# Kernel tuning notes

Hardware: AMD Instinct MI355X
Metric: run time of the kernel (lower is better)

Reference implementation:

```python
import jax, jax.numpy as jnp
import numpy as np

GROUPS = 4
EPS = 1e-5


def conv1d(x, w, b):
    # x [B,Cin,NA,T], w [Cout,Cin,1,K], 'same' padding along T
    K = w.shape[-1]
    pad = (K - 1) // 2
    y = jax.lax.conv_general_dilated(x, w, (1, 1), [(0, 0), (pad, pad)],
                                     dimension_numbers=('NCHW', 'OIHW', 'NCHW'))
    return y + b[None, :, None, None]


def group_norm(x, g, b):
    B, C, H, W = x.shape
    xg = x.reshape(B, GROUPS, C // GROUPS, H, W)
    m = xg.mean((2, 3, 4), keepdims=True)
    v = xg.var((2, 3, 4), keepdims=True)
    xn = ((xg - m) * jax.lax.rsqrt(v + EPS)).reshape(B, C, H, W)
    return xn * g[None, :, None, None] + b[None, :, None, None]


def avg_pool_t(x, k):
    B, C, H, T = x.shape
    return x.reshape(B, C, H, T // k, k).mean(-1)


def branch(x, w1, b1, g1, be1, w2, b2, g2, be2):
    y = avg_pool_t(jax.nn.gelu(group_norm(conv1d(x, w1, b1), g1, be1), approximate=False), 2)
    y = avg_pool_t(jax.nn.gelu(group_norm(conv1d(y, w2, b2), g2, be2), approximate=False), 4)
    # B C NA T -> B NA (T C)
    B, C, NA, T = y.shape
    return jnp.transpose(y, (0, 2, 3, 1)).reshape(B, NA, T * C)


def rvq(feat, cbs):
    # feat [B,NA,D]; cbs [nq,V,D] -> residual vector quantization
    def step(res, cb):
        d = (res * res).sum(-1, keepdims=True) \
            - 2.0 * jnp.einsum('bnd,vd->bnv', res, cb) \
            + (cb * cb).sum(-1)              # [B,NA,V]
        idx = jnp.argmin(d, axis=-1)          # [B,NA]
        q = cb[idx]                           # gather [B,NA,D]
        return res - q, (q, idx)
    _, (qs, idxs) = jax.lax.scan(step, feat, cbs)
    return qs.sum(0), idxs                    # [B,NA,D], [nq,B,NA]


def reference(x, w11, w12, w13, w14, b1, g1, be1,
              w21, w22, w23, w24, b2, g2, be2, codebooks):
    B, N, A, T = x.shape
    xc = x.reshape(B, N * A, T)[:, None]  # [B,1,NA,T]
    feats = jnp.stack([
        branch(xc, w11, b1[0], g1[0], be1[0], w21, b2[0], g2[0], be2[0]),
        branch(xc, w12, b1[1], g1[1], be1[1], w22, b2[1], g2[1], be2[1]),
        branch(xc, w13, b1[2], g1[2], be1[2], w23, b2[2], g2[2], be2[2]),
        branch(xc, w14, b1[3], g1[3], be1[3], w24, b2[3], g2[3], be2[3]),
    ])  # [4,B,NA,D]
    quant, idxs = jax.vmap(rvq)(feats, codebooks)  # [4,B,NA,D], [4,nq,B,NA]
    # straight-through estimator
    out = feats + jax.lax.stop_gradient(quant - feats)
    return out, idxs


def setup_inputs() -> dict:
    key = jax.random.key(0)
    ks = jax.random.split(key, 16)
    C = 8
    d = {
        'x': jax.random.normal(ks[0], (8, 32, 4, 200), jnp.float32),
        'w11': jax.random.normal(ks[1], (C, 1, 1, 21), jnp.float32) * 0.1,
        'w12': jax.random.normal(ks[2], (C, 1, 1, 15), jnp.float32) * 0.1,
        'w13': jax.random.normal(ks[3], (C, 1, 1, 9), jnp.float32) * 0.1,
        'w14': jax.random.normal(ks[4], (C, 1, 1, 5), jnp.float32) * 0.1,
        'b1': jnp.zeros((4, C), jnp.float32),
        'g1': jnp.ones((4, C), jnp.float32),
        'be1': jnp.zeros((4, C), jnp.float32),
        'w21': jax.random.normal(ks[5], (C, C, 1, 9), jnp.float32) * 0.1,
        'w22': jax.random.normal(ks[6], (C, C, 1, 7), jnp.float32) * 0.1,
        'w23': jax.random.normal(ks[7], (C, C, 1, 5), jnp.float32) * 0.1,
        'w24': jax.random.normal(ks[8], (C, C, 1, 3), jnp.float32) * 0.1,
        'b2': jnp.zeros((4, C), jnp.float32),
        'g2': jnp.ones((4, C), jnp.float32),
        'be2': jnp.zeros((4, C), jnp.float32),
        'codebooks': jax.random.normal(ks[9], (4, 8, 8192, 200), jnp.float32) * 0.5,
    }
    return d
```

## Files before the change

kernel.cpp:

```cpp
#include <hip/hip_runtime.h>
#include <hip/hip_bf16.h>
#include <math.h>

#define NBR 4
#define BB 8
#define NAA 128
#define T_IN 200
#define CCH 8
#define NQ 8
#define NV 8192
#define DD 200
#define ROWS 1024
#define KPAD 224
#define NKG 28
#define CBQSH ((size_t)NBR*NKG*NV*8)

typedef __attribute__((ext_vector_type(8))) short short8;
typedef __attribute__((ext_vector_type(4))) float f32x4;

__device__ __forceinline__ unsigned short f2bf(float x) {
  unsigned u = __float_as_uint(x);
  unsigned r = (u + 0x7fffu + ((u >> 16) & 1u)) >> 16;
  return (unsigned short)r;
}
__device__ __forceinline__ bool lexlt(float av, int ai, float bv, int bi) {
  return (av < bv) || (av == bv && ai < bi);
}
__device__ __forceinline__ unsigned umn(unsigned a, unsigned b) { return a < b ? a : b; }
__device__ __forceinline__ unsigned umx(unsigned a, unsigned b) { return a > b ? a : b; }
__device__ __forceinline__ unsigned skey(float s, int idx) {
  unsigned u = __float_as_uint(s);
  unsigned mask = ((unsigned)((int)u >> 31)) | 0x80000000u;
  return ((u ^ mask) & 0xFFFFE000u) | (unsigned)idx;
}
__device__ __forceinline__ void gld16(const short* g, short* s) {
  __builtin_amdgcn_global_load_lds(
      (const __attribute__((address_space(1))) unsigned*)g,
      (__attribute__((address_space(3))) unsigned*)s, 16, 0, 0);
}

template<int K>
__device__ __forceinline__ void conv1_stats_body(
    const float* __restrict__ sx, const float* __restrict__ wr, float bias,
    int tl, double& s, double& s2)
{
  constexpr int pad = (K-1)/2;
  if (tl < 25) {
    int t0 = 8*tl;
    float xw[K+7];
    #pragma unroll
    for (int i = 0; i < K+7; ++i) {
      int xi = t0 - pad + i;
      xw[i] = ((unsigned)xi < (unsigned)T_IN) ? sx[xi] : 0.f;
    }
    #pragma unroll
    for (int m = 0; m < 8; ++m) {
      float acc = bias;
      #pragma unroll
      for (int k = 0; k < K; ++k)
        acc = fmaf(wr[k], xw[m + k], acc);
      s += acc; s2 += (double)acc * acc;
    }
  }
}

__global__ __launch_bounds__(256) void k_conv1_stats(
    const float* __restrict__ x,
    const float* __restrict__ w11, const float* __restrict__ w12,
    const float* __restrict__ w13, const float* __restrict__ w14,
    const float* __restrict__ b1,
    double* __restrict__ partS, double* __restrict__ partQ)
{
  const int bid = blockIdx.x;
  const int br = bid >> 10;
  const int b  = (bid >> 7) & 7;
  const int na = bid & 127;
  const int tid = threadIdx.x;
  const int c  = tid >> 5;
  const int tl = tid & 31;
  const float* w = (br==0) ? w11 : (br==1) ? w12 : (br==2) ? w13 : w14;

  __shared__ float sx[T_IN];
  if (tid < T_IN) sx[tid] = x[((size_t)b*NAA + na)*T_IN + tid];
  __syncthreads();

  const float bias = b1[br*CCH + c];
  double s = 0.0, s2 = 0.0;
  switch (br) {
    case 0: conv1_stats_body<21>(sx, w + c*21, bias, tl, s, s2); break;
    case 1: conv1_stats_body<15>(sx, w + c*15, bias, tl, s, s2); break;
    case 2: conv1_stats_body<9> (sx, w + c*9,  bias, tl, s, s2); break;
    default: conv1_stats_body<5>(sx, w + c*5,  bias, tl, s, s2); break;
  }
  __shared__ double rs[256], rq[256];
  rs[tid] = s; rq[tid] = s2;
  __syncthreads();
  for (int off = 32; off > 0; off >>= 1) {
    if ((tid & 63) < off) { rs[tid] += rs[tid+off]; rq[tid] += rq[tid+off]; }
    __syncthreads();
  }
  if ((tid & 63) == 0) {
    int g = tid >> 6;
    int pi = (((br*BB + b)*4 + g) << 7) + na;
    partS[pi] = rs[tid]; partQ[pi] = rq[tid];
  }
}

template<int K1, int K2>
__device__ __forceinline__ void mid_body(
    const float* __restrict__ sx, float* __restrict__ sy,
    const float* __restrict__ w1, const float* __restrict__ w2,
    float bias1, float fm, float rst, float gm, float bt, float bias2,
    int c, int tl, float* __restrict__ yout, double& s, double& s2)
{
  constexpr int pad1 = (K1-1)/2, pad2 = (K2-1)/2;
  const float* wr = w1 + c*K1;
  if (tl < 25) {
    int t0 = 8*tl;
    float xw[K1+7];
    #pragma unroll
    for (int i = 0; i < K1+7; ++i) {
      int xi = t0 - pad1 + i;
      xw[i] = ((unsigned)xi < (unsigned)T_IN) ? sx[xi] : 0.f;
    }
    #pragma unroll
    for (int m = 0; m < 4; ++m) {
      float u = 0.f;
      #pragma unroll
      for (int h = 0; h < 2; ++h) {
        float acc = bias1;
        #pragma unroll
        for (int k = 0; k < K1; ++k)
          acc = fmaf(wr[k], xw[2*m + h + k], acc);
        float xn = (acc - fm) * rst * gm + bt;
        u += 0.5f * xn * (1.0f + erff(xn * 0.70710678118654752440f));
      }
      sy[c*100 + 4*tl + m] = 0.5f * u;
    }
  }
  __syncthreads();
  if (tl < 25) {
    int t0 = 4*tl;
    float a0 = bias2, a1 = bias2, a2 = bias2, a3 = bias2;
    #pragma unroll
    for (int cin = 0; cin < CCH; ++cin) {
      const float* wr2 = w2 + (c*CCH + cin)*K2;
      float wv[K2];
      #pragma unroll
      for (int k = 0; k < K2; ++k) wv[k] = wr2[k];
      float yw[K2+3];
      #pragma unroll
      for (int i = 0; i < K2+3; ++i) {
        int yi = t0 - pad2 + i;
        yw[i] = ((unsigned)yi < 100u) ? sy[cin*100 + yi] : 0.f;
      }
      #pragma unroll
      for (int k = 0; k < K2; ++k) a0 = fmaf(wv[k], yw[k], a0);
      #pragma unroll
      for (int k = 0; k < K2; ++k) a1 = fmaf(wv[k], yw[1 + k], a1);
      #pragma unroll
      for (int k = 0; k < K2; ++k) a2 = fmaf(wv[k], yw[2 + k], a2);
      #pragma unroll
      for (int k = 0; k < K2; ++k) a3 = fmaf(wv[k], yw[3 + k], a3);
    }
    *(float4*)&yout[t0] = make_float4(a0, a1, a2, a3);
    s += a0; s2 += (double)a0 * a0;
    s += a1; s2 += (double)a1 * a1;
    s += a2; s2 += (double)a2 * a2;
    s += a3; s2 += (double)a3 * a3;
  }
}

__global__ __launch_bounds__(256) void k_mid(
    const float* __restrict__ x,
    const float* __restrict__ w11, const float* __restrict__ w12,
    const float* __restrict__ w13, const float* __restrict__ w14,
    const float* __restrict__ b1, const float* __restrict__ g1,
    const float* __restrict__ be1,
    const double* __restrict__ partS1, const double* __restrict__ partQ1,
    const float* __restrict__ w21, const float* __restrict__ w22,
    const float* __restrict__ w23, const float* __restrict__ w24,
    const float* __restrict__ b2,
    float* __restrict__ y2raw,
    double* __restrict__ partS, double* __restrict__ partQ)
{
  const int bid = blockIdx.x;
  const int br = bid >> 10;
  const int b  = (bid >> 7) & 7;
  const int na = bid & 127;
  const int tid = threadIdx.x;
  const int c  = tid >> 5;
  const int tl = tid & 31;
  const int wid = tid >> 6;
  const int l = tid & 63;
  const float* w1 = (br==0) ? w11 : (br==1) ? w12 : (br==2) ? w13 : w14;
  const float* w2 = (br==0) ? w21 : (br==1) ? w22 : (br==2) ? w23 : w24;

  __shared__ float sx[T_IN];
  __shared__ float sy[CCH*100];
  __shared__ float sstat[8];
  if (tid < T_IN) sx[tid] = x[((size_t)b*NAA + na)*T_IN + tid];

  {
    int base = (((br*BB + b)*4 + wid) << 7);
    double a  = partS1[base + l] + partS1[base + 64 + l];
    double qn = partQ1[base + l] + partQ1[base + 64 + l];
    #pragma unroll
    for (int m = 32; m >= 1; m >>= 1) {
      a  += __shfl_xor(a, m);
      qn += __shfl_xor(qn, m);
    }
    if (l == 0) {
      double mean = a / 51200.0;
      double var  = qn / 51200.0 - mean*mean;
      sstat[wid*2]     = (float)mean;
      sstat[wid*2 + 1] = (float)(1.0 / sqrt(var + 1e-5));
    }
  }
  __syncthreads();

  const float bias1 = b1[br*CCH + c];
  const float fm  = sstat[(c>>1)*2];
  const float rst = sstat[(c>>1)*2 + 1];
  const float gm = g1[br*CCH + c], bt = be1[br*CCH + c];
  const float bias2 = b2[br*CCH + c];
  float* yout = y2raw + ((((size_t)br*BB + b)*CCH + c)*NAA + na)*100;

  double s = 0.0, s2 = 0.0;
  switch (br) {
    case 0: mid_body<21,9>(sx, sy, w1, w2, bias1, fm, rst, gm, bt, bias2, c, tl, yout, s, s2); break;
    case 1: mid_body<15,7>(sx, sy, w1, w2, bias1, fm, rst, gm, bt, bias2, c, tl, yout, s, s2); break;
    case 2: mid_body<9,5> (sx, sy, w1, w2, bias1, fm, rst, gm, bt, bias2, c, tl, yout, s, s2); break;
    default: mid_body<5,3>(sx, sy, w1, w2, bias1, fm, rst, gm, bt, bias2, c, tl, yout, s, s2); break;
  }

  __shared__ double rs[256], rq[256];
  rs[tid] = s; rq[tid] = s2;
  __syncthreads();
  for (int off = 32; off > 0; off >>= 1) {
    if ((tid & 63) < off) { rs[tid] += rs[tid+off]; rq[tid] += rq[tid+off]; }
    __syncthreads();
  }
  if ((tid & 63) == 0) {
    int g = tid >> 6;
    int pi = (((br*BB + b)*4 + g) << 7) + na;
    partS[pi] = rs[tid]; partQ[pi] = rq[tid];
  }
}

__global__ __launch_bounds__(256) void k_tail(
    const float* __restrict__ y2raw, const float* __restrict__ g2,
    const float* __restrict__ be2,
    const double* __restrict__ partS2, const double* __restrict__ partQ2,
    float* __restrict__ res, short* __restrict__ resh)
{
  const int tid = threadIdx.x;
  int idx = blockIdx.x * 256 + tid;
  int c  = idx & 7;
  int tp = (idx >> 3) % 25;
  int na = (idx / 200) & 127;
  int b  = (idx / 25600) & 7;
  int br = idx / 204800;
  const int wid = tid >> 6, l = tid & 63;

  if (idx < NBR*3*ROWS*8) {
    int pos = idx & 7;
    int prow = (idx >> 3) & 1023;
    int r2  = idx >> 13;
    int pbr = r2 / 3, kgp = r2 - pbr*3;
    resh[(((size_t)pbr*NKG + 25 + kgp)*ROWS + prow)*8 + pos] = 0;
  }

  __shared__ float sstat[8];
  {
    int base = (((br*BB + b)*4 + wid) << 7);
    double a  = partS2[base + l] + partS2[base + 64 + l];
    double qn = partQ2[base + l] + partQ2[base + 64 + l];
    #pragma unroll
    for (int m = 32; m >= 1; m >>= 1) {
      a  += __shfl_xor(a, m);
      qn += __shfl_xor(qn, m);
    }
    if (l == 0) {
      double mean = a / 25600.0;
      double var  = qn / 25600.0 - mean*mean;
      sstat[wid*2]     = (float)mean;
      sstat[wid*2 + 1] = (float)(1.0 / sqrt(var + 1e-5));
    }
  }
  __syncthreads();

  int g = c >> 1;
  float fm  = sstat[g*2];
  float rst = sstat[g*2 + 1];
  float gm = g2[br*CCH + c], bt = be2[br*CCH + c];
  float4 v = *(const float4*)&y2raw[((((size_t)br*BB + b)*CCH + c)*NAA + na)*100 + 4*tp];
  float sum4 = 0.f;
  #pragma unroll
  for (int h = 0; h < 4; ++h) {
    float xv = (h==0) ? v.x : (h==1) ? v.y : (h==2) ? v.z : v.w;
    float xn = (xv - fm) * rst * gm + bt;
    sum4 += 0.5f * xn * (1.0f + erff(xn * 0.70710678118654752440f));
  }
  float val = 0.25f * sum4;
  int row = b*NAA + na;
  res[((size_t)br*ROWS + row)*DD + tp*8 + c] = val;
  resh[(((size_t)br*NKG + tp)*ROWS + row)*8 + c] = (short)f2bf(val);
}

__global__ __launch_bounds__(256) void k_cvt_cb(
    const float* __restrict__ cbs, int q0, int nq,
    short* __restrict__ dh, float* __restrict__ cbn)
{
  __shared__ short S[25][65][8];
  const int blk = blockIdx.x;
  const int vt = blk & 127;
  const int t  = blk >> 7;
  const int br = t / nq, ql = t - br*nq;
  const int q = q0 + ql;
  const int tid = threadIdx.x;
  const int row = tid >> 2, fq = tid & 3;
  const int v0 = vt*64;
  const float* srow = cbs + ((size_t)(br*NQ + q)*NV + v0 + row)*DD;

  float s = 0.f;
  for (int j = 0; j < 13; ++j) {
    int f4 = fq + 4*j;
    if (f4 < 50) {
      float4 f = *(const float4*)&srow[4*f4];
      s += f.x*f.x + f.y*f.y + f.z*f.z + f.w*f.w;
      *(short4*)&S[f4>>1][row][(f4&1)*4] =
          make_short4((short)f2bf(f.x), (short)f2bf(f.y),
                      (short)f2bf(f.z), (short)f2bf(f.w));
    }
  }
  s += __shfl_xor(s, 1);
  s += __shfl_xor(s, 2);
  if (fq == 0) cbn[(size_t)(br*NQ + q)*NV + v0 + row] = s;
  __syncthreads();

  short* dq = dh + (size_t)ql*CBQSH;
  for (int u = tid; u < NKG*64*2; u += 256) {
    int kg = u >> 7;
    int rem = u & 127;
    int v = rem >> 1, pos = (rem & 1)*4;
    short4 val = (kg < 25) ? *(const short4*)&S[kg][v][pos]
                           : make_short4(0,0,0,0);
    *(short4*)&dq[(((size_t)br*NKG + kg)*NV + v0 + v)*8 + pos] = val;
  }
}

__global__ __launch_bounds__(256) void k_gemm(
    const short* __restrict__ resh, const short* __restrict__ cbh,
    const float* __restrict__ cbn, int q,
    unsigned* __restrict__ candk)
{
  __shared__ short S[2][4][130][8];

  const int p = blockIdx.x;
  const int x = p & 7;
  const int sIdx = p >> 3;
  const int br = sIdx >> 6;
  const int rb = (sIdx >> 3) & 7;
  const int vb = x*8 + (sIdx & 7);
  const int tid = threadIdx.x;
  const int w = tid >> 6;
  const int l = tid & 63;
  const int wr = w >> 1, wc = w & 1;
  const int kgl = l >> 4, fr = l & 15;

  f32x4 acc[4][4];
  #pragma unroll
  for (int i = 0; i < 4; ++i)
    #pragma unroll
    for (int j = 0; j < 4; ++j)
      acc[i][j] = (f32x4){0.f, 0.f, 0.f, 0.f};

  short8 aA[2][4];

  #define STAGE(nb, ks)                                                         \
    {                                                                           \
      _Pragma("unroll")                                                         \
      for (int i = 0; i < 4; ++i)                                               \
        aA[nb][i] = *(const short8*)&resh[                                      \
          (((size_t)br*NKG + (ks)*4 + kgl)*ROWS + rb*128 + wr*64 + i*16 + fr)*8]; \
      _Pragma("unroll")                                                         \
      for (int t = 0; t < 2; ++t) {                                             \
        int u = (w << 1) | t;                                                   \
        int kg = u >> 1, wh = u & 1;                                            \
        gld16(cbh + (((size_t)br*NKG + (ks)*4 + kg)*NV + vb*128 + wh*64 + l)*8, \
              &S[nb][kg][wh*64][0]);                                            \
      }                                                                         \
    }

  STAGE(0, 0);

  #pragma unroll
  for (int ks = 0; ks < 7; ++ks) {
    const int cur = ks & 1, nxt = cur ^ 1;
    if (ks < 6) {
      STAGE(nxt, ks + 1);
      asm volatile("s_waitcnt vmcnt(6)" ::: "memory");
    } else {
      asm volatile("s_waitcnt vmcnt(0)" ::: "memory");
    }
    __builtin_amdgcn_s_barrier();

    short8 bh[4];
    #pragma unroll
    for (int j = 0; j < 4; ++j)
      bh[j] = *(const short8*)&S[cur][kgl][wc*64 + j*16 + fr][0];
    #pragma unroll
    for (int i = 0; i < 4; ++i)
      #pragma unroll
      for (int j = 0; j < 4; ++j)
        acc[i][j] = __builtin_amdgcn_mfma_f32_16x16x32_bf16(aA[cur][i], bh[j], acc[i][j], 0, 0, 0);

    asm volatile("" ::: "memory");
    __builtin_amdgcn_s_barrier();
  }

  const float* cn = cbn + (size_t)(br*NQ + q)*NV;
  float nj[4]; int vgj[4];
  #pragma unroll
  for (int j = 0; j < 4; ++j) {
    vgj[j] = vb*128 + wc*64 + j*16 + fr;
    nj[j] = 0.5f * cn[vgj[j]];
  }
  #pragma unroll
  for (int i = 0; i < 4; ++i) {
    #pragma unroll
    for (int reg = 0; reg < 4; ++reg) {
      unsigned k0 = skey(nj[0] - acc[i][0][reg], vgj[0]);
      unsigned k1 = skey(nj[1] - acc[i][1][reg], vgj[1]);
      unsigned k2 = skey(nj[2] - acc[i][2][reg], vgj[2]);
      unsigned k3 = skey(nj[3] - acc[i][3][reg], vgj[3]);
      unsigned a = umn(k0, k1), b = umx(k0, k1);
      unsigned c = umn(k2, k3), d = umx(k2, k3);
      unsigned c1 = umn(a, c);
      unsigned c2 = umn(umx(a, c), umn(b, d));
      #pragma unroll
      for (int m = 1; m <= 8; m <<= 1) {
        unsigned o1 = __shfl_xor(c1, m);
        unsigned o2 = __shfl_xor(c2, m);
        unsigned t = umx(c1, o1);
        c1 = umn(c1, o1);
        c2 = umn(umn(t, c2), o2);
      }
      if (fr == 0) {
        int grow = br*ROWS + rb*128 + wr*64 + i*16 + kgl*4 + reg;
        size_t o = ((size_t)grow*64 + vb)*4 + wc*2;
        candk[o] = c1; candk[o+1] = c2;
      }
    }
  }
  #undef STAGE
}

__global__ __launch_bounds__(256) void k_update3(
    const float* __restrict__ cbs, const float* __restrict__ cbn,
    const unsigned* __restrict__ candk,
    float* __restrict__ res, float* __restrict__ outq,
    float* __restrict__ outi, short* __restrict__ resh, int q)
{
  const int wid = threadIdx.x >> 6;
  const int lane = threadIdx.x & 63;
  const int r = blockIdx.x*4 + wid;
  const int br = r >> 10;
  const int row = r & 1023;

  const unsigned* ck = candk + (size_t)r * 256;
  uint4 kk = *(const uint4*)&ck[4*lane];
  unsigned c0 = kk.x, c1 = kk.y, c2 = kk.z, c3 = kk.w;

  unsigned mykey = 0xFFFFFFFFu;
  #pragma unroll
  for (int t = 0; t < 8; ++t) {
    unsigned lm = umn(umn(c0, c1), umn(c2, c3));
    #pragma unroll
    for (int m = 1; m <= 32; m <<= 1)
      lm = umn(lm, __shfl_xor(lm, m));
    if (c0 == lm) c0 = 0xFFFFFFFFu;
    if (c1 == lm) c1 = 0xFFFFFFFFu;
    if (c2 == lm) c2 = 0xFFFFFFFFu;
    if (c3 == lm) c3 = 0xFFFFFFFFu;
    if ((lane >> 3) == t) mykey = lm;
  }
  const int mycand = (int)(mykey & 0x1FFFu);

  const int kl = lane & 7;
  const float* cbrow = cbs + ((size_t)(br*NQ + q)*NV + mycand)*DD;
  const float* rrow0 = res + (size_t)r*DD;
  float dot = 0.f;
  #pragma unroll
  for (int u = 0; u < 7; ++u) {
    int f4 = kl + 8*u;
    if (f4 < 50) {
      float4 r4 = *(const float4*)&rrow0[4*f4];
      float4 c4 = *(const float4*)&cbrow[4*f4];
      dot = fmaf(r4.x, c4.x, dot);
      dot = fmaf(r4.y, c4.y, dot);
      dot = fmaf(r4.z, c4.z, dot);
      dot = fmaf(r4.w, c4.w, dot);
    }
  }
  dot += __shfl_xor(dot, 1);
  dot += __shfl_xor(dot, 2);
  dot += __shfl_xor(dot, 4);
  float dist = fmaf(-2.f, dot, cbn[(size_t)(br*NQ + q)*NV + mycand]);

  float bv = dist; int bi = mycand;
  #pragma unroll
  for (int m = 8; m <= 32; m <<= 1) {
    float ov = __shfl_xor(bv, m); int oi = __shfl_xor(bi, m);
    if (lexlt(ov, oi, bv, bi)) { bv = ov; bi = oi; }
  }

  if (lane == 0)
    outi[(((size_t)br*NQ + q)*BB + (row >> 7))*NAA + (row & 127)] = (float)bi;

  const float* c = cbs + ((size_t)(br*NQ + q)*NV + bi)*DD;
  float* rrow = res  + ((size_t)br*ROWS + row)*DD;
  float* qrow = outq + ((size_t)br*ROWS + row)*DD;
  if (lane < 50) {
    float4 cvv = *(const float4*)&c[4*lane];
    float4 r4 = *(const float4*)&rrow[4*lane];
    r4.x -= cvv.x; r4.y -= cvv.y; r4.z -= cvv.z; r4.w -= cvv.w;
    *(float4*)&rrow[4*lane] = r4;
    float4 qv;
    if (q == 0) {
      qv = cvv;
    } else {
      qv = *(const float4*)&qrow[4*lane];
      qv.x += cvv.x; qv.y += cvv.y; qv.z += cvv.z; qv.w += cvv.w;
    }
    *(float4*)&qrow[4*lane] = qv;

    *(short4*)&resh[(((size_t)br*NKG + (lane>>1))*ROWS + row)*8 + (lane&1)*4] =
        make_short4((short)f2bf(r4.x), (short)f2bf(r4.y),
                    (short)f2bf(r4.z), (short)f2bf(r4.w));
  }
}

extern "C" void kernel_launch(void* const* d_in, const int* in_sizes, int n_in,
                              void* d_out, int out_size, void* d_ws, size_t ws_size,
                              hipStream_t stream)
{
  const float* x   = (const float*)d_in[0];
  const float* w11 = (const float*)d_in[1];
  const float* w12 = (const float*)d_in[2];
  const float* w13 = (const float*)d_in[3];
  const float* w14 = (const float*)d_in[4];
  const float* b1  = (const float*)d_in[5];
  const float* g1  = (const float*)d_in[6];
  const float* be1 = (const float*)d_in[7];
  const float* w21 = (const float*)d_in[8];
  const float* w22 = (const float*)d_in[9];
  const float* w23 = (const float*)d_in[10];
  const float* w24 = (const float*)d_in[11];
  const float* b2  = (const float*)d_in[12];
  const float* g2  = (const float*)d_in[13];
  const float* be2 = (const float*)d_in[14];
  const float* cbs = (const float*)d_in[15];

  char* wsb = (char*)d_ws;
  double* partS1 = (double*)wsb;
  double* partQ1 = partS1 + 16384;
  double* partS2 = partQ1 + 16384;
  double* partQ2 = partS2 + 16384;
  float* fbase = (float*)(partQ2 + 16384);
  float* y2raw = fbase;
  float* res   = y2raw + 3276800;
  float* cbn   = res + 819200;
  unsigned* candk = (unsigned*)(cbn + 262144);
  short* resh  = (short*)(candk + 1048576);
  short* cbh   = resh + 917504;
  const size_t base_bytes = (char*)cbh - wsb;
  const bool big = ws_size >= base_bytes + CBQSH*8*sizeof(short) + 1024;

  float* outq = (float*)d_out;
  float* outi = outq + 819200;

  k_conv1_stats<<<4096, 256, 0, stream>>>(x, w11, w12, w13, w14, b1, partS1, partQ1);
  k_mid<<<4096, 256, 0, stream>>>(x, w11, w12, w13, w14, b1, g1, be1,
                                  partS1, partQ1,
                                  w21, w22, w23, w24, b2, y2raw, partS2, partQ2);
  k_tail<<<3200, 256, 0, stream>>>(y2raw, g2, be2, partS2, partQ2, res, resh);

  if (big)
    k_cvt_cb<<<NBR*NQ*128, 256, 0, stream>>>(cbs, 0, NQ, cbh, cbn);

  for (int q = 0; q < NQ; ++q) {
    if (!big)
      k_cvt_cb<<<NBR*128, 256, 0, stream>>>(cbs, q, 1, cbh, cbn);
    const short* cbh_q = cbh + (big ? (size_t)q*CBQSH : 0);
    k_gemm<<<2048, 256, 0, stream>>>(resh, cbh_q, cbn, q, candk);
    k_update3<<<1024, 256, 0, stream>>>(cbs, cbn, candk, res, outq, outi, resh, q);
  }
}
```

Before: 429.0 us.

## Fuse codebook bf16 conversion into front-end conv kernels as extra blocks

```diff
diff --git a/kernel.cpp b/kernel.cpp
--- a/kernel.cpp
+++ b/kernel.cpp
@@ -39,6 +39,46 @@
       (__attribute__((address_space(3))) unsigned*)s, 16, 0, 0);
 }
 
+__device__ __forceinline__ void cvt_body(
+    int cvtblk, int q0, const float* __restrict__ cbs,
+    short* __restrict__ dh, float* __restrict__ cbn, short (*S)[65][8])
+{
+  const int vt = cvtblk & 127;
+  const int t  = cvtblk >> 7;
+  const int br = t >> 2, qr = t & 3;
+  const int q = q0 + qr;
+  const int tid = threadIdx.x;
+  const int row = tid >> 2, fq = tid & 3;
+  const int v0 = vt*64;
+  const float* srow = cbs + ((size_t)(br*NQ + q)*NV + v0 + row)*DD;
+
+  float s = 0.f;
+  for (int j = 0; j < 13; ++j) {
+    int f4 = fq + 4*j;
+    if (f4 < 50) {
+      float4 f = *(const float4*)&srow[4*f4];
+      s += f.x*f.x + f.y*f.y + f.z*f.z + f.w*f.w;
+      *(short4*)&S[f4>>1][row][(f4&1)*4] =
+          make_short4((short)f2bf(f.x), (short)f2bf(f.y),
+                      (short)f2bf(f.z), (short)f2bf(f.w));
+    }
+  }
+  s += __shfl_xor(s, 1);
+  s += __shfl_xor(s, 2);
+  if (fq == 0) cbn[(size_t)(br*NQ + q)*NV + v0 + row] = s;
+  __syncthreads();
+
+  short* dq = dh + (size_t)q*CBQSH;
+  for (int u = tid; u < NKG*64*2; u += 256) {
+    int kg = u >> 7;
+    int rem = u & 127;
+    int v = rem >> 1, pos = (rem & 1)*4;
+    short4 val = (kg < 25) ? *(const short4*)&S[kg][v][pos]
+                           : make_short4(0,0,0,0);
+    *(short4*)&dq[(((size_t)br*NKG + kg)*NV + v0 + v)*8 + pos] = val;
+  }
+}
+
 template<int K>
 __device__ __forceinline__ void conv1_stats_body(
     const float* __restrict__ sx, const float* __restrict__ wr, float bias,
@@ -61,6 +101,57 @@
         acc = fmaf(wr[k], xw[m + k], acc);
       s += acc; s2 += (double)acc * acc;
     }
+  }
+}
+
+__global__ __launch_bounds__(256) void k_front1(
+    const float* __restrict__ x,
+    const float* __restrict__ w11, const float* __restrict__ w12,
+    const float* __restrict__ w13, const float* __restrict__ w14,
+    const float* __restrict__ b1,
+    double* __restrict__ partS, double* __restrict__ partQ,
+    const float* __restrict__ cbs, short* __restrict__ dh,
+    float* __restrict__ cbn)
+{
+  __shared__ float sx[T_IN];
+  __shared__ double rs[256], rq[256];
+  __shared__ short S[25][65][8];
+  const int bid = blockIdx.x;
+  const int tid = threadIdx.x;
+
+  if (bid >= 4096) {
+    cvt_body(bid - 4096, 0, cbs, dh, cbn, S);
+    return;
+  }
+
+  const int br = bid >> 10;
+  const int b  = (bid >> 7) & 7;
+  const int na = bid & 127;
+  const int c  = tid >> 5;
+  const int tl = tid & 31;
+  const float* w = (br==0) ? w11 : (br==1) ? w12 : (br==2) ? w13 : w14;
+
+  if (tid < T_IN) sx[tid] = x[((size_t)b*NAA + na)*T_IN + tid];
+  __syncthreads();
+
+  const float bias = b1[br*CCH + c];
+  double s = 0.0, s2 = 0.0;
+  switch (br) {
+    case 0: conv1_stats_body<21>(sx, w + c*21, bias, tl, s, s2); break;
+    case 1: conv1_stats_body<15>(sx, w + c*15, bias, tl, s, s2); break;
+    case 2: conv1_stats_body<9> (sx, w + c*9,  bias, tl, s, s2); break;
+    default: conv1_stats_body<5>(sx, w + c*5,  bias, tl, s, s2); break;
+  }
+  rs[tid] = s; rq[tid] = s2;
+  __syncthreads();
+  for (int off = 32; off > 0; off >>= 1) {
+    if ((tid & 63) < off) { rs[tid] += rs[tid+off]; rq[tid] += rq[tid+off]; }
+    __syncthreads();
+  }
+  if ((tid & 63) == 0) {
+    int g = tid >> 6;
+    int pi = (((br*BB + b)*4 + g) << 7) + na;
+    partS[pi] = rs[tid]; partQ[pi] = rq[tid];
   }
 }
 
@@ -182,13 +273,27 @@
     const float* __restrict__ w23, const float* __restrict__ w24,
     const float* __restrict__ b2,
     float* __restrict__ y2raw,
-    double* __restrict__ partS, double* __restrict__ partQ)
-{
+    double* __restrict__ partS, double* __restrict__ partQ,
+    const float* __restrict__ cbs, short* __restrict__ dh,
+    float* __restrict__ cbn)
+{
+  __shared__ float sx[T_IN];
+  __shared__ float sy[CCH*100];
+  __shared__ float sstat[8];
+  __shared__ double rs[256], rq[256];
+  __shared__ short S[25][65][8];
+
   const int bid = blockIdx.x;
+  const int tid = threadIdx.x;
+
+  if (bid >= 4096) {
+    cvt_body(bid - 4096, 4, cbs, dh, cbn, S);
+    return;
+  }
+
   const int br = bid >> 10;
   const int b  = (bid >> 7) & 7;
   const int na = bid & 127;
-  const int tid = threadIdx.x;
   const int c  = tid >> 5;
   const int tl = tid & 31;
   const int wid = tid >> 6;
@@ -196,9 +301,6 @@
   const float* w1 = (br==0) ? w11 : (br==1) ? w12 : (br==2) ? w13 : w14;
   const float* w2 = (br==0) ? w21 : (br==1) ? w22 : (br==2) ? w23 : w24;
 
-  __shared__ float sx[T_IN];
-  __shared__ float sy[CCH*100];
-  __shared__ float sstat[8];
   if (tid < T_IN) sx[tid] = x[((size_t)b*NAA + na)*T_IN + tid];
 
   {
@@ -234,7 +336,6 @@
     default: mid_body<5,3>(sx, sy, w1, w2, bias1, fm, rst, gm, bt, bias2, c, tl, yout, s, s2); break;
   }
 
-  __shared__ double rs[256], rq[256];
   rs[tid] = s; rq[tid] = s2;
   __syncthreads();
   for (int off = 32; off > 0; off >>= 1) {
@@ -309,15 +410,13 @@
 }
 
 __global__ __launch_bounds__(256) void k_cvt_cb(
-    const float* __restrict__ cbs, int q0, int nq,
+    const float* __restrict__ cbs, int q,
     short* __restrict__ dh, float* __restrict__ cbn)
 {
   __shared__ short S[25][65][8];
   const int blk = blockIdx.x;
   const int vt = blk & 127;
-  const int t  = blk >> 7;
-  const int br = t / nq, ql = t - br*nq;
-  const int q = q0 + ql;
+  const int br = blk >> 7;
   const int tid = threadIdx.x;
   const int row = tid >> 2, fq = tid & 3;
   const int v0 = vt*64;
@@ -339,14 +438,13 @@
   if (fq == 0) cbn[(size_t)(br*NQ + q)*NV + v0 + row] = s;
   __syncthreads();
 
-  short* dq = dh + (size_t)ql*CBQSH;
   for (int u = tid; u < NKG*64*2; u += 256) {
     int kg = u >> 7;
     int rem = u & 127;
     int v = rem >> 1, pos = (rem & 1)*4;
     short4 val = (kg < 25) ? *(const short4*)&S[kg][v][pos]
                            : make_short4(0,0,0,0);
-    *(short4*)&dq[(((size_t)br*NKG + kg)*NV + v0 + v)*8 + pos] = val;
+    *(short4*)&dh[(((size_t)br*NKG + kg)*NV + v0 + v)*8 + pos] = val;
   }
 }
 
@@ -581,18 +679,25 @@
   float* outq = (float*)d_out;
   float* outi = outq + 819200;
 
-  k_conv1_stats<<<4096, 256, 0, stream>>>(x, w11, w12, w13, w14, b1, partS1, partQ1);
-  k_mid<<<4096, 256, 0, stream>>>(x, w11, w12, w13, w14, b1, g1, be1,
-                                  partS1, partQ1,
-                                  w21, w22, w23, w24, b2, y2raw, partS2, partQ2);
+  if (big) {
+    k_front1<<<4096 + 2048, 256, 0, stream>>>(x, w11, w12, w13, w14, b1,
+                                              partS1, partQ1, cbs, cbh, cbn);
+    k_mid<<<4096 + 2048, 256, 0, stream>>>(x, w11, w12, w13, w14, b1, g1, be1,
+                                           partS1, partQ1,
+                                           w21, w22, w23, w24, b2, y2raw,
+                                           partS2, partQ2, cbs, cbh, cbn);
+  } else {
+    k_conv1_stats<<<4096, 256, 0, stream>>>(x, w11, w12, w13, w14, b1, partS1, partQ1);
+    k_mid<<<4096, 256, 0, stream>>>(x, w11, w12, w13, w14, b1, g1, be1,
+                                    partS1, partQ1,
+                                    w21, w22, w23, w24, b2, y2raw,
+                                    partS2, partQ2, cbs, cbh, cbn);
+  }
   k_tail<<<3200, 256, 0, stream>>>(y2raw, g2, be2, partS2, partQ2, res, resh);
-
-  if (big)
-    k_cvt_cb<<<NBR*NQ*128, 256, 0, stream>>>(cbs, 0, NQ, cbh, cbn);
 
   for (int q = 0; q < NQ; ++q) {
     if (!big)
-      k_cvt_cb<<<NBR*128, 256, 0, stream>>>(cbs, q, 1, cbh, cbn);
+      k_cvt_cb<<<NBR*128, 256, 0, stream>>>(cbs, q, cbh, cbn);
     const short* cbh_q = cbh + (big ? (size_t)q*CBQSH : 0);
     k_gemm<<<2048, 256, 0, stream>>>(resh, cbh_q, cbn, q, candk);
     k_update3<<<1024, 256, 0, stream>>>(cbs, cbn, candk, res, outq, outi, resh, q);
```

After: 427.3 us. Within noise of the previous version (-0.4%).
